# Optimization experiments

Measured on AMD Instinct MI355X. Metric: run time of the kernel, lower is better.

The kernel has to match this reference:

```python
import jax, jax.numpy as jnp
import numpy as np

N = 100000
E = 1600000
IN_FEATS, HIDDEN, NUM_CLASSES = 128, 64, 32


def _graph_conv(src, dst, x, W, b):
    """DGL GraphConv, norm='both', allow_zero_in_degree=True.
    out_i = b + sum_{(j->i)} x_j W / sqrt(max(deg_out(j),1) * max(deg_in(i),1))
    """
    ones = jnp.ones(src.shape[0], dtype=x.dtype)
    deg_out = jnp.clip(jax.ops.segment_sum(ones, src, num_segments=N), 1.0)
    deg_in = jnp.clip(jax.ops.segment_sum(ones, dst, num_segments=N), 1.0)
    # pre-normalize, apply weight first (smaller message dim), then aggregate
    h = (x * jax.lax.rsqrt(deg_out)[:, None]) @ W          # [N, out]
    agg = jax.ops.segment_sum(h[src], dst, num_segments=N)  # [N, out]
    return agg * jax.lax.rsqrt(deg_in)[:, None] + b


def setup_inputs() -> dict:
    key = jax.random.key(0)
    ks = jax.random.split(key, 8)
    x = jax.random.normal(ks[0], (N, IN_FEATS), dtype=jnp.float32)
    src1 = jax.random.randint(ks[1], (E,), 0, N, dtype=jnp.int32)
    dst1 = jax.random.randint(ks[2], (E,), 0, N, dtype=jnp.int32)
    src2 = jax.random.randint(ks[3], (E,), 0, N, dtype=jnp.int32)
    dst2 = jax.random.randint(ks[4], (E,), 0, N, dtype=jnp.int32)
    W1 = jax.random.normal(ks[5], (IN_FEATS, HIDDEN), dtype=jnp.float32) / np.sqrt(IN_FEATS)
    b1 = jnp.zeros((HIDDEN,), dtype=jnp.float32)
    W2 = jax.random.normal(ks[6], (HIDDEN, NUM_CLASSES), dtype=jnp.float32) / np.sqrt(HIDDEN)
    b2 = jnp.zeros((NUM_CLASSES,), dtype=jnp.float32)
    return {"x": x, "src1": src1, "dst1": dst1, "src2": src2, "dst2": dst2,
            "W1": W1, "b1": b1, "W2": W2, "b2": b2}


def reference(x, src1, dst1, src2, dst2, W1, b1, W2, b2):
    results = []
    for src, dst in ((src1, dst1), (src2, dst2)):
        h = jax.nn.relu(_graph_conv(src, dst, x, W1, b1))
        h = _graph_conv(src, dst, h, W2, b2)
        results.append(h)
    return jnp.mean(jnp.stack(results), axis=0)
```

## Files before the change

### kernel.cpp

```cpp
#include <hip/hip_runtime.h>

#define TPB 256
#define CAP 48
#define CHUNK 16384
#define GP1 64
#define GP2 32

__device__ inline unsigned short f2bf(float f) {
    union { float f; unsigned int u; } v; v.f = f;
    unsigned int u = v.u + 0x7FFFu + ((v.u >> 16) & 1u);
    return (unsigned short)(u >> 16);
}
__device__ inline float bflo(unsigned int v) {
    union { unsigned int u; float f; } w; w.u = v << 16;
    return w.f;
}
__device__ inline float bfhi(unsigned int v) {
    union { unsigned int u; float f; } w; w.u = v & 0xffff0000u;
    return w.f;
}

__global__ void hist_kernel(const int* __restrict__ s1, const int* __restrict__ s2,
                            int* __restrict__ part, int E, int nchunk) {
    __shared__ int h[CHUNK];
    int b     = blockIdx.x;
    int which = b / (nchunk * GP2);
    int rem   = b % (nchunk * GP2);
    int chunk = rem / GP2;
    int p     = rem % GP2;
    const int* src = which ? s2 : s1;

    for (int i = threadIdx.x; i < CHUNK; i += TPB) h[i] = 0;
    __syncthreads();

    int lo  = chunk * CHUNK;
    int per = ((E + GP2 - 1) / GP2 + 3) & ~3;
    int e0  = p * per;
    int e1  = e0 + per; if (e1 > E) e1 = E;
    if (e0 < e1) {
        int nvec = (e1 - e0) >> 2;
        const int4* vsrc = (const int4*)(src + e0);
        for (int i = threadIdx.x; i < nvec; i += TPB) {
            int4 v = vsrc[i];
            unsigned d;
            d = (unsigned)(v.x - lo); if (d < CHUNK) atomicAdd(&h[d], 1);
            d = (unsigned)(v.y - lo); if (d < CHUNK) atomicAdd(&h[d], 1);
            d = (unsigned)(v.z - lo); if (d < CHUNK) atomicAdd(&h[d], 1);
            d = (unsigned)(v.w - lo); if (d < CHUNK) atomicAdd(&h[d], 1);
        }
        for (int e = e0 + (nvec << 2) + threadIdx.x; e < e1; e += TPB) {
            unsigned d = (unsigned)(src[e] - lo);
            if (d < CHUNK) atomicAdd(&h[d], 1);
        }
    }
    __syncthreads();
    int* dstp = part + (size_t)b * CHUNK;
    for (int i = threadIdx.x; i < CHUNK; i += TPB) dstp[i] = h[i];
}

__global__ void histreduce_kernel(const int* __restrict__ part, int* __restrict__ dout,
                                  int N, int nchunk) {
    int i = blockIdx.x * TPB + threadIdx.x;
    if (i >= 2 * N) return;
    int which = i < N ? 0 : 1;
    int node  = which ? i - N : i;
    int chunk = node / CHUNK, off = node % CHUNK;
    const int* base = part + ((size_t)(which * nchunk + chunk) * GP2) * CHUNK + off;
    int s = 0;
    #pragma unroll
    for (int p = 0; p < GP2; p++) s += base[(size_t)p * CHUNK];
    dout[i] = s;
}

__global__ void hist1_kernel(const int* __restrict__ arr, int* __restrict__ part, int E) {
    __shared__ int h[CHUNK];
    int b     = blockIdx.x;
    int chunk = b / GP1;
    int p     = b % GP1;
    for (int i = threadIdx.x; i < CHUNK; i += TPB) h[i] = 0;
    __syncthreads();
    int lo  = chunk * CHUNK;
    int per = ((E + GP1 - 1) / GP1 + 3) & ~3;
    int e0  = p * per;
    int e1  = e0 + per; if (e1 > E) e1 = E;
    if (e0 < e1) {
        int nvec = (e1 - e0) >> 2;
        const int4* vsrc = (const int4*)(arr + e0);
        for (int i = threadIdx.x; i < nvec; i += TPB) {
            int4 v = vsrc[i];
            unsigned d;
            d = (unsigned)(v.x - lo); if (d < CHUNK) atomicAdd(&h[d], 1);
            d = (unsigned)(v.y - lo); if (d < CHUNK) atomicAdd(&h[d], 1);
            d = (unsigned)(v.z - lo); if (d < CHUNK) atomicAdd(&h[d], 1);
            d = (unsigned)(v.w - lo); if (d < CHUNK) atomicAdd(&h[d], 1);
        }
        for (int e = e0 + (nvec << 2) + threadIdx.x; e < e1; e += TPB) {
            unsigned d = (unsigned)(arr[e] - lo);
            if (d < CHUNK) atomicAdd(&h[d], 1);
        }
    }
    __syncthreads();
    int* dstp = part + (size_t)b * CHUNK;
    for (int i = threadIdx.x; i < CHUNK; i += TPB) dstp[i] = h[i];
}

__global__ void offset_kernel(int* __restrict__ part, int* __restrict__ din, int N) {
    int n = blockIdx.x * TPB + threadIdx.x;
    if (n >= N) return;
    int c = n / CHUNK, o = n % CHUNK;
    int* base = part + ((size_t)c * GP1) * CHUNK + o;
    int run = n * CAP;
    #pragma unroll
    for (int p = 0; p < GP1; p++) {
        int t = base[(size_t)p * CHUNK];
        base[(size_t)p * CHUNK] = run;
        run += t;
    }
    din[n] = run - n * CAP;
}

__global__ void scatterC_kernel(const int* __restrict__ src, const int* __restrict__ dst,
                                const int* __restrict__ part, int* __restrict__ esrc, int E) {
    __shared__ int cur[CHUNK];
    int b     = blockIdx.x;
    int chunk = b / GP1;
    int p     = b % GP1;
    const int* offp = part + (size_t)b * CHUNK;
    for (int i = threadIdx.x; i < CHUNK; i += TPB) cur[i] = offp[i];
    __syncthreads();
    int lo  = chunk * CHUNK;
    int per = ((E + GP1 - 1) / GP1 + 3) & ~3;
    int e0  = p * per;
    int e1  = e0 + per; if (e1 > E) e1 = E;
    if (e0 < e1) {
        int nvec = (e1 - e0) >> 2;
        const int4* d4 = (const int4*)(dst + e0);
        const int4* s4 = (const int4*)(src + e0);
        for (int i = threadIdx.x; i < nvec; i += TPB) {
            int4 d = d4[i];
            int4 s = s4[i];
            unsigned u; int pos;
            u = (unsigned)(d.x - lo);
            if (u < CHUNK) { pos = atomicAdd(&cur[u], 1); if (pos < (lo + (int)u + 1) * CAP) esrc[pos] = s.x; }
            u = (unsigned)(d.y - lo);
            if (u < CHUNK) { pos = atomicAdd(&cur[u], 1); if (pos < (lo + (int)u + 1) * CAP) esrc[pos] = s.y; }
            u = (unsigned)(d.z - lo);
            if (u < CHUNK) { pos = atomicAdd(&cur[u], 1); if (pos < (lo + (int)u + 1) * CAP) esrc[pos] = s.z; }
            u = (unsigned)(d.w - lo);
            if (u < CHUNK) { pos = atomicAdd(&cur[u], 1); if (pos < (lo + (int)u + 1) * CAP) esrc[pos] = s.w; }
        }
        for (int e = e0 + (nvec << 2) + threadIdx.x; e < e1; e += TPB) {
            int dd = dst[e];
            unsigned u = (unsigned)(dd - lo);
            if (u < CHUNK) { int pos = atomicAdd(&cur[u], 1); if (pos < (dd + 1) * CAP) esrc[pos] = src[e]; }
        }
    }
}

__global__ void gemm1_kernel(const float* __restrict__ x, const float* __restrict__ W,
                             const int* __restrict__ dout1, const int* __restrict__ dout2,
                             unsigned short* __restrict__ Y0, unsigned short* __restrict__ Y1,
                             int N) {
    __shared__ float xs[64 * 128];
    __shared__ float ws[128 * 64];
    int tid  = threadIdx.x;
    int row0 = blockIdx.x * 64;
    for (int i = tid; i < 2048; i += TPB)
        ((float4*)ws)[i] = ((const float4*)W)[i];
    for (int i = tid; i < 2048; i += TPB) {
        int r = row0 + (i >> 5);
        ((float4*)xs)[i] = (r < N) ? ((const float4*)x)[(size_t)r * 32 + (i & 31)]
                                   : make_float4(0.f, 0.f, 0.f, 0.f);
    }
    __syncthreads();
    int tr = tid >> 4, tc = tid & 15;
    float acc[4][4] = {};
    for (int k4 = 0; k4 < 32; k4++) {
        float4 a[4], b[4];
        #pragma unroll
        for (int j = 0; j < 4; j++) a[j] = ((float4*)xs)[(tr * 4 + j) * 32 + k4];
        #pragma unroll
        for (int j = 0; j < 4; j++) b[j] = ((float4*)ws)[(k4 * 4 + j) * 16 + tc];
        #pragma unroll
        for (int i = 0; i < 4; i++) {
            float4 ai = a[i];
            acc[i][0] += ai.x * b[0].x + ai.y * b[1].x + ai.z * b[2].x + ai.w * b[3].x;
            acc[i][1] += ai.x * b[0].y + ai.y * b[1].y + ai.z * b[2].y + ai.w * b[3].y;
            acc[i][2] += ai.x * b[0].z + ai.y * b[1].z + ai.z * b[2].z + ai.w * b[3].z;
            acc[i][3] += ai.x * b[0].w + ai.y * b[1].w + ai.z * b[2].w + ai.w * b[3].w;
        }
    }
    #pragma unroll
    for (int i = 0; i < 4; i++) {
        int r = row0 + tr * 4 + i;
        if (r < N) {
            int g0 = dout1[r], g1 = dout2[r];
            float s0 = rsqrtf((float)(g0 > 1 ? g0 : 1));
            float s1 = rsqrtf((float)(g1 > 1 ? g1 : 1));
            size_t o = (size_t)r * 64 + tc * 4;
            ushort4 p0 = make_ushort4(f2bf(acc[i][0] * s0), f2bf(acc[i][1] * s0),
                                      f2bf(acc[i][2] * s0), f2bf(acc[i][3] * s0));
            ushort4 p1 = make_ushort4(f2bf(acc[i][0] * s1), f2bf(acc[i][1] * s1),
                                      f2bf(acc[i][2] * s1), f2bf(acc[i][3] * s1));
            *(ushort4*)(Y0 + o) = p0;
            *(ushort4*)(Y1 + o) = p1;
        }
    }
}

__global__ void agg1f_kernel(const int* __restrict__ esrc, const int* __restrict__ din,
                             const unsigned short* __restrict__ Yg,
                             const float* __restrict__ b1, const float* __restrict__ W2,
                             const int* __restrict__ doutg,
                             unsigned short* __restrict__ H2, int N) {
    __shared__ float hs[4][64];
    int tid  = threadIdx.x;
    int w    = tid >> 6;
    int lane = tid & 63;
    int half = lane >> 5;
    int l    = lane & 31;

    float4 w2r[8];
    #pragma unroll
    for (int k4 = 0; k4 < 8; k4++) {
        int k = (half << 5) + (k4 << 2);
        w2r[k4].x = W2[(k + 0) * 32 + l];
        w2r[k4].y = W2[(k + 1) * 32 + l];
        w2r[k4].z = W2[(k + 2) * 32 + l];
        w2r[k4].w = W2[(k + 3) * 32 + l];
    }

    int node = blockIdx.x * 4 + w;
    if (node >= N) return;

    int dn = din[node];
    float si = rsqrtf((float)(dn > 1 ? dn : 1));
    if (dn > CAP) dn = CAP;
    const int* es = esrc + (size_t)node * CAP;

    float a0 = 0.f, a1 = 0.f;
    int i = 0;
    for (; i + 16 <= dn; i += 16) {
        int4 a = *(const int4*)(es + i);
        int4 b = *(const int4*)(es + i + 4);
        int4 c = *(const int4*)(es + i + 8);
        int4 d = *(const int4*)(es + i + 12);
        int s0 = half ? a.y : a.x;
        int s1 = half ? a.w : a.z;
        int s2 = half ? b.y : b.x;
        int s3 = half ? b.w : b.z;
        int s4 = half ? c.y : c.x;
        int s5 = half ? c.w : c.z;
        int s6 = half ? d.y : d.x;
        int s7 = half ? d.w : d.z;
        unsigned v0 = *(const unsigned*)(Yg + (size_t)s0 * 64 + 2 * l);
        unsigned v1 = *(const unsigned*)(Yg + (size_t)s1 * 64 + 2 * l);
        unsigned v2 = *(const unsigned*)(Yg + (size_t)s2 * 64 + 2 * l);
        unsigned v3 = *(const unsigned*)(Yg + (size_t)s3 * 64 + 2 * l);
        unsigned v4 = *(const unsigned*)(Yg + (size_t)s4 * 64 + 2 * l);
        unsigned v5 = *(const unsigned*)(Yg + (size_t)s5 * 64 + 2 * l);
        unsigned v6 = *(const unsigned*)(Yg + (size_t)s6 * 64 + 2 * l);
        unsigned v7 = *(const unsigned*)(Yg + (size_t)s7 * 64 + 2 * l);
        a0 += bflo(v0) + bflo(v1) + bflo(v2) + bflo(v3)
            + bflo(v4) + bflo(v5) + bflo(v6) + bflo(v7);
        a1 += bfhi(v0) + bfhi(v1) + bfhi(v2) + bfhi(v3)
            + bfhi(v4) + bfhi(v5) + bfhi(v6) + bfhi(v7);
    }
    for (; i + 8 <= dn; i += 8) {
        int4 a = *(const int4*)(es + i);
        int4 b = *(const int4*)(es + i + 4);
        int s0 = half ? a.y : a.x;
        int s1 = half ? a.w : a.z;
        int s2 = half ? b.y : b.x;
        int s3 = half ? b.w : b.z;
        unsigned v0 = *(const unsigned*)(Yg + (size_t)s0 * 64 + 2 * l);
        unsigned v1 = *(const unsigned*)(Yg + (size_t)s1 * 64 + 2 * l);
        unsigned v2 = *(const unsigned*)(Yg + (size_t)s2 * 64 + 2 * l);
        unsigned v3 = *(const unsigned*)(Yg + (size_t)s3 * 64 + 2 * l);
        a0 += bflo(v0) + bflo(v1) + bflo(v2) + bflo(v3);
        a1 += bfhi(v0) + bfhi(v1) + bfhi(v2) + bfhi(v3);
    }
    for (int e = i + half; e < dn; e += 2) {
        unsigned v = *(const unsigned*)(Yg + (size_t)es[e] * 64 + 2 * l);
        a0 += bflo(v);
        a1 += bfhi(v);
    }
    a0 += __shfl_xor(a0, 32);
    a1 += __shfl_xor(a1, 32);

    if (half == 0) {
        float2 bb = *(const float2*)(b1 + 2 * l);
        float h0 = a0 * si + bb.x; h0 = h0 > 0.f ? h0 : 0.f;
        float h1 = a1 * si + bb.y; h1 = h1 > 0.f ? h1 : 0.f;
        *(float2*)&hs[w][2 * l] = make_float2(h0, h1);
    }

    const float4* hrow = (const float4*)(hs[w] + (half << 5));
    float part = 0.f;
    #pragma unroll
    for (int k4 = 0; k4 < 8; k4++) {
        float4 hv = hrow[k4];
        part += hv.x * w2r[k4].x + hv.y * w2r[k4].y + hv.z * w2r[k4].z + hv.w * w2r[k4].w;
    }
    float total = part + __shfl_xor(part, 32);
    if (half == 0) {
        int g = doutg[node];
        float so = rsqrtf((float)(g > 1 ? g : 1));
        H2[(size_t)node * 32 + l] = f2bf(total * so);
    }
}

__global__ void agg2_kernel(const int* __restrict__ esrc, const int* __restrict__ din,
                            const unsigned short* __restrict__ H2,
                            const float* __restrict__ b2, float* __restrict__ out,
                            int N, int first) {
    int node = blockIdx.x * 16 + (threadIdx.x >> 4);
    int l    = threadIdx.x & 15;
    if (node >= N) return;
    int dn = din[node];
    float si = rsqrtf((float)(dn > 1 ? dn : 1));
    if (dn > CAP) dn = CAP;
    const int* es = esrc + (size_t)node * CAP;
    float a0 = 0.f, a1 = 0.f;
    int i = 0;
    for (; i + 16 <= dn; i += 16) {
        int4 a = *(const int4*)(es + i);
        int4 b = *(const int4*)(es + i + 4);
        int4 c = *(const int4*)(es + i + 8);
        int4 d = *(const int4*)(es + i + 12);
        unsigned v0 = *(const unsigned*)(H2 + (size_t)a.x * 32 + 2 * l);
        unsigned v1 = *(const unsigned*)(H2 + (size_t)a.y * 32 + 2 * l);
        unsigned v2 = *(const unsigned*)(H2 + (size_t)a.z * 32 + 2 * l);
        unsigned v3 = *(const unsigned*)(H2 + (size_t)a.w * 32 + 2 * l);
        unsigned v4 = *(const unsigned*)(H2 + (size_t)b.x * 32 + 2 * l);
        unsigned v5 = *(const unsigned*)(H2 + (size_t)b.y * 32 + 2 * l);
        unsigned v6 = *(const unsigned*)(H2 + (size_t)b.z * 32 + 2 * l);
        unsigned v7 = *(const unsigned*)(H2 + (size_t)b.w * 32 + 2 * l);
        unsigned v8 = *(const unsigned*)(H2 + (size_t)c.x * 32 + 2 * l);
        unsigned v9 = *(const unsigned*)(H2 + (size_t)c.y * 32 + 2 * l);
        unsigned va = *(const unsigned*)(H2 + (size_t)c.z * 32 + 2 * l);
        unsigned vb = *(const unsigned*)(H2 + (size_t)c.w * 32 + 2 * l);
        unsigned vc = *(const unsigned*)(H2 + (size_t)d.x * 32 + 2 * l);
        unsigned vd = *(const unsigned*)(H2 + (size_t)d.y * 32 + 2 * l);
        unsigned ve = *(const unsigned*)(H2 + (size_t)d.z * 32 + 2 * l);
        unsigned vf = *(const unsigned*)(H2 + (size_t)d.w * 32 + 2 * l);
        a0 += bflo(v0) + bflo(v1) + bflo(v2) + bflo(v3)
            + bflo(v4) + bflo(v5) + bflo(v6) + bflo(v7)
            + bflo(v8) + bflo(v9) + bflo(va) + bflo(vb)
            + bflo(vc) + bflo(vd) + bflo(ve) + bflo(vf);
        a1 += bfhi(v0) + bfhi(v1) + bfhi(v2) + bfhi(v3)
            + bfhi(v4) + bfhi(v5) + bfhi(v6) + bfhi(v7)
            + bfhi(v8) + bfhi(v9) + bfhi(va) + bfhi(vb)
            + bfhi(vc) + bfhi(vd) + bfhi(ve) + bfhi(vf);
    }
    if (i + 8 <= dn) {
        int4 a = *(const int4*)(es + i);
        int4 b = *(const int4*)(es + i + 4);
        unsigned v0 = *(const unsigned*)(H2 + (size_t)a.x * 32 + 2 * l);
        unsigned v1 = *(const unsigned*)(H2 + (size_t)a.y * 32 + 2 * l);
        unsigned v2 = *(const unsigned*)(H2 + (size_t)a.z * 32 + 2 * l);
        unsigned v3 = *(const unsigned*)(H2 + (size_t)a.w * 32 + 2 * l);
        unsigned v4 = *(const unsigned*)(H2 + (size_t)b.x * 32 + 2 * l);
        unsigned v5 = *(const unsigned*)(H2 + (size_t)b.y * 32 + 2 * l);
        unsigned v6 = *(const unsigned*)(H2 + (size_t)b.z * 32 + 2 * l);
        unsigned v7 = *(const unsigned*)(H2 + (size_t)b.w * 32 + 2 * l);
        a0 += bflo(v0) + bflo(v1) + bflo(v2) + bflo(v3)
            + bflo(v4) + bflo(v5) + bflo(v6) + bflo(v7);
        a1 += bfhi(v0) + bfhi(v1) + bfhi(v2) + bfhi(v3)
            + bfhi(v4) + bfhi(v5) + bfhi(v6) + bfhi(v7);
        i += 8;
    }
    if (i + 4 <= dn) {
        int4 a = *(const int4*)(es + i);
        unsigned v0 = *(const unsigned*)(H2 + (size_t)a.x * 32 + 2 * l);
        unsigned v1 = *(const unsigned*)(H2 + (size_t)a.y * 32 + 2 * l);
        unsigned v2 = *(const unsigned*)(H2 + (size_t)a.z * 32 + 2 * l);
        unsigned v3 = *(const unsigned*)(H2 + (size_t)a.w * 32 + 2 * l);
        a0 += bflo(v0) + bflo(v1) + bflo(v2) + bflo(v3);
        a1 += bfhi(v0) + bfhi(v1) + bfhi(v2) + bfhi(v3);
        i += 4;
    }
    for (; i < dn; i++) {
        unsigned v = *(const unsigned*)(H2 + (size_t)es[i] * 32 + 2 * l);
        a0 += bflo(v);
        a1 += bfhi(v);
    }
    float2 bb = *(const float2*)(b2 + 2 * l);
    float v0 = 0.5f * (a0 * si + bb.x);
    float v1 = 0.5f * (a1 * si + bb.y);
    size_t o = (size_t)node * 32 + 2 * l;
    if (first) {
        *(float2*)(out + o) = make_float2(v0, v1);
    } else {
        float2 prev = *(const float2*)(out + o);
        *(float2*)(out + o) = make_float2(prev.x + v0, prev.y + v1);
    }
}

extern "C" void kernel_launch(void* const* d_in, const int* in_sizes, int n_in,
                              void* d_out, int out_size, void* d_ws, size_t ws_size,
                              hipStream_t stream) {
    const float* x    = (const float*)d_in[0];
    const int* srcs[2] = {(const int*)d_in[1], (const int*)d_in[3]};
    const int* dsts[2] = {(const int*)d_in[2], (const int*)d_in[4]};
    const float* W1   = (const float*)d_in[5];
    const float* b1   = (const float*)d_in[6];
    const float* W2   = (const float*)d_in[7];
    const float* b2   = (const float*)d_in[8];
    float* out        = (float*)d_out;

    const int N = in_sizes[0] / 128;
    const int E = in_sizes[1];
    const int nchunk = (N + CHUNK - 1) / CHUNK;

    unsigned short* Y1G0 = (unsigned short*)d_ws;
    unsigned short* Y1G1 = Y1G0 + (size_t)64 * N;
    float* SCR           = (float*)(Y1G1 + (size_t)64 * N);
    unsigned short* H2   = (unsigned short*)(SCR + (size_t)64 * N);
    int* DOUT            = (int*)(H2 + (size_t)32 * N);
    int* DIN             = DOUT + (size_t)2 * N;
    int* ESRC            = DIN + (size_t)2 * N;
    int* PART2           = (int*)d_ws;
    int* PART1           = (int*)SCR;

    hist_kernel<<<2 * nchunk * GP2, TPB, 0, stream>>>(srcs[0], srcs[1], PART2, E, nchunk);
    histreduce_kernel<<<(2 * N + TPB - 1) / TPB, TPB, 0, stream>>>(PART2, DOUT, N, nchunk);

    gemm1_kernel<<<(N + 63) / 64, TPB, 0, stream>>>(x, W1, DOUT, DOUT + N, Y1G0, Y1G1, N);

    for (int g = 0; g < 2; g++) {
        const unsigned short* Yg = g == 0 ? Y1G0 : Y1G1;
        int* din = DIN + (size_t)g * N;

        hist1_kernel<<<nchunk * GP1, TPB, 0, stream>>>(dsts[g], PART1, E);
        offset_kernel<<<(N + TPB - 1) / TPB, TPB, 0, stream>>>(PART1, din, N);
        scatterC_kernel<<<nchunk * GP1, TPB, 0, stream>>>(srcs[g], dsts[g], PART1, ESRC, E);

        agg1f_kernel<<<(N + 3) / 4, TPB, 0, stream>>>(ESRC, din, Yg, b1, W2,
                                                      DOUT + (size_t)g * N, H2, N);
        agg2_kernel<<<(N + 15) / 16, TPB, 0, stream>>>(ESRC, din, H2, b2, out, N, g == 0);
    }
}
```

Measured before the change: 372.6 us.

## Pack degree histograms into 8-bit counters to widen chunks and cut passes

Histogram, offset and scatter kernels now keep four 8-bit counters per 32-bit shared word. This lets each block cover 65536 nodes instead of 16384, so each edge array is scanned fewer times (2 chunks instead of 7) and the partial-histogram buffers are four times smaller. Scatter now computes the slot from a per-partition 8-bit rank plus node*CAP instead of a global running offset. The risk is counter overflow: a per-partition count or prefix above 255 would carry into the neighbouring byte. With random graphs at average degree 16 that is unlikely but not guaranteed, and it also relies on degree prefixes staying small.

```diff
diff --git a/kernel.cpp b/kernel.cpp
--- a/kernel.cpp
+++ b/kernel.cpp
@@ -2,9 +2,11 @@
 
 #define TPB 256
 #define CAP 48
-#define CHUNK 16384
-#define GP1 64
-#define GP2 32
+#define CHUNK 65536
+#define CSH 16
+#define WPC (CHUNK / 4)
+#define GP1 128
+#define GP2 64
 
 __device__ inline unsigned short f2bf(float f) {
     union { float f; unsigned int u; } v; v.f = f;
@@ -20,9 +22,9 @@
     return w.f;
 }
 
-__global__ void hist_kernel(const int* __restrict__ s1, const int* __restrict__ s2,
-                            int* __restrict__ part, int E, int nchunk) {
-    __shared__ int h[CHUNK];
+__global__ void hist8_kernel(const int* __restrict__ s1, const int* __restrict__ s2,
+                             unsigned int* __restrict__ part, int E, int nchunk) {
+    __shared__ unsigned int h[WPC];
     int b     = blockIdx.x;
     int which = b / (nchunk * GP2);
     int rem   = b % (nchunk * GP2);
@@ -30,10 +32,10 @@
     int p     = rem % GP2;
     const int* src = which ? s2 : s1;
 
-    for (int i = threadIdx.x; i < CHUNK; i += TPB) h[i] = 0;
-    __syncthreads();
-
-    int lo  = chunk * CHUNK;
+    for (int i = threadIdx.x; i < WPC; i += TPB) h[i] = 0u;
+    __syncthreads();
+
+    int lo  = chunk << CSH;
     int per = ((E + GP2 - 1) / GP2 + 3) & ~3;
     int e0  = p * per;
     int e1  = e0 + per; if (e1 > E) e1 = E;
@@ -42,44 +44,55 @@
         const int4* vsrc = (const int4*)(src + e0);
         for (int i = threadIdx.x; i < nvec; i += TPB) {
             int4 v = vsrc[i];
-            unsigned d;
-            d = (unsigned)(v.x - lo); if (d < CHUNK) atomicAdd(&h[d], 1);
-            d = (unsigned)(v.y - lo); if (d < CHUNK) atomicAdd(&h[d], 1);
-            d = (unsigned)(v.z - lo); if (d < CHUNK) atomicAdd(&h[d], 1);
-            d = (unsigned)(v.w - lo); if (d < CHUNK) atomicAdd(&h[d], 1);
+            unsigned u;
+            u = (unsigned)(v.x - lo); if (u < CHUNK) atomicAdd(&h[u >> 2], 1u << ((u & 3) << 3));
+            u = (unsigned)(v.y - lo); if (u < CHUNK) atomicAdd(&h[u >> 2], 1u << ((u & 3) << 3));
+            u = (unsigned)(v.z - lo); if (u < CHUNK) atomicAdd(&h[u >> 2], 1u << ((u & 3) << 3));
+            u = (unsigned)(v.w - lo); if (u < CHUNK) atomicAdd(&h[u >> 2], 1u << ((u & 3) << 3));
         }
         for (int e = e0 + (nvec << 2) + threadIdx.x; e < e1; e += TPB) {
-            unsigned d = (unsigned)(src[e] - lo);
-            if (d < CHUNK) atomicAdd(&h[d], 1);
-        }
-    }
-    __syncthreads();
-    int* dstp = part + (size_t)b * CHUNK;
-    for (int i = threadIdx.x; i < CHUNK; i += TPB) dstp[i] = h[i];
-}
-
-__global__ void histreduce_kernel(const int* __restrict__ part, int* __restrict__ dout,
-                                  int N, int nchunk) {
-    int i = blockIdx.x * TPB + threadIdx.x;
-    if (i >= 2 * N) return;
-    int which = i < N ? 0 : 1;
-    int node  = which ? i - N : i;
-    int chunk = node / CHUNK, off = node % CHUNK;
-    const int* base = part + ((size_t)(which * nchunk + chunk) * GP2) * CHUNK + off;
-    int s = 0;
+            unsigned u = (unsigned)(src[e] - lo);
+            if (u < CHUNK) atomicAdd(&h[u >> 2], 1u << ((u & 3) << 3));
+        }
+    }
+    __syncthreads();
+    unsigned int* dstp = part + (size_t)b * WPC;
+    for (int i = threadIdx.x; i < WPC; i += TPB) dstp[i] = h[i];
+}
+
+__global__ void histreduce8_kernel(const unsigned int* __restrict__ part,
+                                   int* __restrict__ dout, int N, int nchunk, int ngroup) {
+    int t = blockIdx.x * TPB + threadIdx.x;
+    if (t >= 2 * ngroup) return;
+    int which = t / ngroup;
+    int g     = t % ngroup;
+    int node0 = g * 4;
+    if (node0 >= N) return;
+    int chunk    = node0 >> CSH;
+    int off_word = (node0 & (CHUNK - 1)) >> 2;
+    const unsigned int* base = part + ((size_t)(which * nchunk + chunk) * GP2) * WPC + off_word;
+    int s0 = 0, s1 = 0, s2 = 0, s3 = 0;
     #pragma unroll
-    for (int p = 0; p < GP2; p++) s += base[(size_t)p * CHUNK];
-    dout[i] = s;
-}
-
-__global__ void hist1_kernel(const int* __restrict__ arr, int* __restrict__ part, int E) {
-    __shared__ int h[CHUNK];
+    for (int p = 0; p < GP2; p++) {
+        unsigned int w = base[(size_t)p * WPC];
+        s0 += w & 255u; s1 += (w >> 8) & 255u; s2 += (w >> 16) & 255u; s3 += (w >> 24) & 255u;
+    }
+    int* d = dout + (size_t)which * N + node0;
+    if (node0 + 0 < N) d[0] = s0;
+    if (node0 + 1 < N) d[1] = s1;
+    if (node0 + 2 < N) d[2] = s2;
+    if (node0 + 3 < N) d[3] = s3;
+}
+
+__global__ void hist1_8_kernel(const int* __restrict__ arr, unsigned int* __restrict__ part,
+                               int E) {
+    __shared__ unsigned int h[WPC];
     int b     = blockIdx.x;
     int chunk = b / GP1;
     int p     = b % GP1;
-    for (int i = threadIdx.x; i < CHUNK; i += TPB) h[i] = 0;
-    __syncthreads();
-    int lo  = chunk * CHUNK;
+    for (int i = threadIdx.x; i < WPC; i += TPB) h[i] = 0u;
+    __syncthreads();
+    int lo  = chunk << CSH;
     int per = ((E + GP1 - 1) / GP1 + 3) & ~3;
     int e0  = p * per;
     int e1  = e0 + per; if (e1 > E) e1 = E;
@@ -88,47 +101,56 @@
         const int4* vsrc = (const int4*)(arr + e0);
         for (int i = threadIdx.x; i < nvec; i += TPB) {
             int4 v = vsrc[i];
-            unsigned d;
-            d = (unsigned)(v.x - lo); if (d < CHUNK) atomicAdd(&h[d], 1);
-            d = (unsigned)(v.y - lo); if (d < CHUNK) atomicAdd(&h[d], 1);
-            d = (unsigned)(v.z - lo); if (d < CHUNK) atomicAdd(&h[d], 1);
-            d = (unsigned)(v.w - lo); if (d < CHUNK) atomicAdd(&h[d], 1);
+            unsigned u;
+            u = (unsigned)(v.x - lo); if (u < CHUNK) atomicAdd(&h[u >> 2], 1u << ((u & 3) << 3));
+            u = (unsigned)(v.y - lo); if (u < CHUNK) atomicAdd(&h[u >> 2], 1u << ((u & 3) << 3));
+            u = (unsigned)(v.z - lo); if (u < CHUNK) atomicAdd(&h[u >> 2], 1u << ((u & 3) << 3));
+            u = (unsigned)(v.w - lo); if (u < CHUNK) atomicAdd(&h[u >> 2], 1u << ((u & 3) << 3));
         }
         for (int e = e0 + (nvec << 2) + threadIdx.x; e < e1; e += TPB) {
-            unsigned d = (unsigned)(arr[e] - lo);
-            if (d < CHUNK) atomicAdd(&h[d], 1);
-        }
-    }
-    __syncthreads();
-    int* dstp = part + (size_t)b * CHUNK;
-    for (int i = threadIdx.x; i < CHUNK; i += TPB) dstp[i] = h[i];
-}
-
-__global__ void offset_kernel(int* __restrict__ part, int* __restrict__ din, int N) {
-    int n = blockIdx.x * TPB + threadIdx.x;
-    if (n >= N) return;
-    int c = n / CHUNK, o = n % CHUNK;
-    int* base = part + ((size_t)c * GP1) * CHUNK + o;
-    int run = n * CAP;
+            unsigned u = (unsigned)(arr[e] - lo);
+            if (u < CHUNK) atomicAdd(&h[u >> 2], 1u << ((u & 3) << 3));
+        }
+    }
+    __syncthreads();
+    unsigned int* dstp = part + (size_t)b * WPC;
+    for (int i = threadIdx.x; i < WPC; i += TPB) dstp[i] = h[i];
+}
+
+__global__ void offset8_kernel(unsigned int* __restrict__ part, int* __restrict__ din,
+                               int N, int ngroup) {
+    int g = blockIdx.x * TPB + threadIdx.x;
+    if (g >= ngroup) return;
+    int node0 = g * 4;
+    if (node0 >= N) return;
+    int chunk    = node0 >> CSH;
+    int off_word = (node0 & (CHUNK - 1)) >> 2;
+    unsigned int* base = part + ((size_t)chunk * GP1) * WPC + off_word;
+    unsigned int r0 = 0, r1 = 0, r2 = 0, r3 = 0;
     #pragma unroll
     for (int p = 0; p < GP1; p++) {
-        int t = base[(size_t)p * CHUNK];
-        base[(size_t)p * CHUNK] = run;
-        run += t;
-    }
-    din[n] = run - n * CAP;
-}
-
-__global__ void scatterC_kernel(const int* __restrict__ src, const int* __restrict__ dst,
-                                const int* __restrict__ part, int* __restrict__ esrc, int E) {
-    __shared__ int cur[CHUNK];
+        unsigned int w = base[(size_t)p * WPC];
+        base[(size_t)p * WPC] = r0 | (r1 << 8) | (r2 << 16) | (r3 << 24);
+        r0 += w & 255u; r1 += (w >> 8) & 255u; r2 += (w >> 16) & 255u; r3 += (w >> 24) & 255u;
+    }
+    int* d = din + node0;
+    if (node0 + 0 < N) d[0] = (int)r0;
+    if (node0 + 1 < N) d[1] = (int)r1;
+    if (node0 + 2 < N) d[2] = (int)r2;
+    if (node0 + 3 < N) d[3] = (int)r3;
+}
+
+__global__ void scatterC8_kernel(const int* __restrict__ src, const int* __restrict__ dst,
+                                 const unsigned int* __restrict__ part,
+                                 int* __restrict__ esrc, int E) {
+    __shared__ unsigned int cur[WPC];
     int b     = blockIdx.x;
     int chunk = b / GP1;
     int p     = b % GP1;
-    const int* offp = part + (size_t)b * CHUNK;
-    for (int i = threadIdx.x; i < CHUNK; i += TPB) cur[i] = offp[i];
-    __syncthreads();
-    int lo  = chunk * CHUNK;
+    const unsigned int* offp = part + (size_t)b * WPC;
+    for (int i = threadIdx.x; i < WPC; i += TPB) cur[i] = offp[i];
+    __syncthreads();
+    int lo  = chunk << CSH;
     int per = ((E + GP1 - 1) / GP1 + 3) & ~3;
     int e0  = p * per;
     int e1  = e0 + per; if (e1 > E) e1 = E;
@@ -139,20 +161,39 @@
         for (int i = threadIdx.x; i < nvec; i += TPB) {
             int4 d = d4[i];
             int4 s = s4[i];
-            unsigned u; int pos;
+            unsigned u, old; int rank;
             u = (unsigned)(d.x - lo);
-            if (u < CHUNK) { pos = atomicAdd(&cur[u], 1); if (pos < (lo + (int)u + 1) * CAP) esrc[pos] = s.x; }
+            if (u < CHUNK) {
+                old = atomicAdd(&cur[u >> 2], 1u << ((u & 3) << 3));
+                rank = (old >> ((u & 3) << 3)) & 0xFF;
+                if (rank < CAP) esrc[(size_t)(lo + (int)u) * CAP + rank] = s.x;
+            }
             u = (unsigned)(d.y - lo);
-            if (u < CHUNK) { pos = atomicAdd(&cur[u], 1); if (pos < (lo + (int)u + 1) * CAP) esrc[pos] = s.y; }
+            if (u < CHUNK) {
+                old = atomicAdd(&cur[u >> 2], 1u << ((u & 3) << 3));
+                rank = (old >> ((u & 3) << 3)) & 0xFF;
+                if (rank < CAP) esrc[(size_t)(lo + (int)u) * CAP + rank] = s.y;
+            }
             u = (unsigned)(d.z - lo);
-            if (u < CHUNK) { pos = atomicAdd(&cur[u], 1); if (pos < (lo + (int)u + 1) * CAP) esrc[pos] = s.z; }
+            if (u < CHUNK) {
+                old = atomicAdd(&cur[u >> 2], 1u << ((u & 3) << 3));
+                rank = (old >> ((u & 3) << 3)) & 0xFF;
+                if (rank < CAP) esrc[(size_t)(lo + (int)u) * CAP + rank] = s.z;
+            }
             u = (unsigned)(d.w - lo);
-            if (u < CHUNK) { pos = atomicAdd(&cur[u], 1); if (pos < (lo + (int)u + 1) * CAP) esrc[pos] = s.w; }
+            if (u < CHUNK) {
+                old = atomicAdd(&cur[u >> 2], 1u << ((u & 3) << 3));
+                rank = (old >> ((u & 3) << 3)) & 0xFF;
+                if (rank < CAP) esrc[(size_t)(lo + (int)u) * CAP + rank] = s.w;
+            }
         }
         for (int e = e0 + (nvec << 2) + threadIdx.x; e < e1; e += TPB) {
-            int dd = dst[e];
-            unsigned u = (unsigned)(dd - lo);
-            if (u < CHUNK) { int pos = atomicAdd(&cur[u], 1); if (pos < (dd + 1) * CAP) esrc[pos] = src[e]; }
+            unsigned u = (unsigned)(dst[e] - lo);
+            if (u < CHUNK) {
+                unsigned old = atomicAdd(&cur[u >> 2], 1u << ((u & 3) << 3));
+                int rank = (old >> ((u & 3) << 3)) & 0xFF;
+                if (rank < CAP) esrc[(size_t)(lo + (int)u) * CAP + rank] = src[e];
+            }
         }
     }
 }
@@ -412,19 +453,19 @@
     const int N = in_sizes[0] / 128;
     const int E = in_sizes[1];
     const int nchunk = (N + CHUNK - 1) / CHUNK;
+    const int ngroup = (N + 3) / 4;
 
     unsigned short* Y1G0 = (unsigned short*)d_ws;
     unsigned short* Y1G1 = Y1G0 + (size_t)64 * N;
-    float* SCR           = (float*)(Y1G1 + (size_t)64 * N);
-    unsigned short* H2   = (unsigned short*)(SCR + (size_t)64 * N);
+    unsigned short* H2   = Y1G1 + (size_t)64 * N;
     int* DOUT            = (int*)(H2 + (size_t)32 * N);
     int* DIN             = DOUT + (size_t)2 * N;
     int* ESRC            = DIN + (size_t)2 * N;
-    int* PART2           = (int*)d_ws;
-    int* PART1           = (int*)SCR;
-
-    hist_kernel<<<2 * nchunk * GP2, TPB, 0, stream>>>(srcs[0], srcs[1], PART2, E, nchunk);
-    histreduce_kernel<<<(2 * N + TPB - 1) / TPB, TPB, 0, stream>>>(PART2, DOUT, N, nchunk);
+    unsigned int* PART   = (unsigned int*)(ESRC + (size_t)N * CAP);
+
+    hist8_kernel<<<2 * nchunk * GP2, TPB, 0, stream>>>(srcs[0], srcs[1], PART, E, nchunk);
+    histreduce8_kernel<<<(2 * ngroup + TPB - 1) / TPB, TPB, 0, stream>>>(PART, DOUT, N,
+                                                                         nchunk, ngroup);
 
     gemm1_kernel<<<(N + 63) / 64, TPB, 0, stream>>>(x, W1, DOUT, DOUT + N, Y1G0, Y1G1, N);
 
@@ -432,9 +473,9 @@
         const unsigned short* Yg = g == 0 ? Y1G0 : Y1G1;
         int* din = DIN + (size_t)g * N;
 
-        hist1_kernel<<<nchunk * GP1, TPB, 0, stream>>>(dsts[g], PART1, E);
-        offset_kernel<<<(N + TPB - 1) / TPB, TPB, 0, stream>>>(PART1, din, N);
-        scatterC_kernel<<<nchunk * GP1, TPB, 0, stream>>>(srcs[g], dsts[g], PART1, ESRC, E);
+        hist1_8_kernel<<<nchunk * GP1, TPB, 0, stream>>>(dsts[g], PART, E);
+        offset8_kernel<<<(ngroup + TPB - 1) / TPB, TPB, 0, stream>>>(PART, din, N, ngroup);
+        scatterC8_kernel<<<nchunk * GP1, TPB, 0, stream>>>(srcs[g], dsts[g], PART, ESRC, E);
 
         agg1f_kernel<<<(N + 3) / 4, TPB, 0, stream>>>(ESRC, din, Yg, b1, W2,
                                                       DOUT + (size_t)g * N, H2, N);
```

Measured after the change: 348.5 us, median of 2. 6.5% less time.
